# Kernel tuning notes

Hardware: AMD Instinct MI355X
Metric: run time of the kernel (lower is better)

Reference implementation:

```python
import jax, jax.numpy as jnp
import numpy as np

D, M, R, N = 64, 256, 3, 1024
L_MID = 2  # number of middle phi layers (L=4 total)


def sp10(x):
    # torch.nn.Softplus(beta=10)
    return jax.nn.softplus(10.0 * x) / 10.0


def setup_inputs() -> dict:
    key = jax.random.key(0)
    ks = jax.random.split(key, 16)
    w_scale = 1.0 / np.sqrt(R)
    a_ht_scale = 0.1 / np.sqrt(M)
    inp = {
        "X": jax.random.uniform(ks[0], (N, D), dtype=jnp.float32),
        "w_first": 1.0 * jax.random.normal(ks[1], (D, M, 1, R), dtype=jnp.float32),
        "w_mid": w_scale * jax.random.normal(ks[2], (L_MID, D, M, R, R), dtype=jnp.float32),
        "w_last": w_scale * jax.random.normal(ks[3], (D, M, R, 1), dtype=jnp.float32),
        "b_first": 0.1 * jax.random.normal(ks[4], (D, M, R), dtype=jnp.float32),
        "b_mid": 0.1 * jax.random.normal(ks[5], (L_MID, D, M, R), dtype=jnp.float32),
        "b_last": 0.1 * jax.random.normal(ks[6], (D, M, 1), dtype=jnp.float32),
        "a_first": jax.random.normal(ks[7], (D, M, R), dtype=jnp.float32),
        "a_mid": jax.random.normal(ks[8], (L_MID, D, M, R), dtype=jnp.float32),
    }
    # HT mixing matrices: init m*eye(m) per group (as in source) + small noise
    dims = [32, 16, 8, 4, 2]
    for i, g in enumerate(dims):
        eye = M * jnp.eye(M, dtype=jnp.float32)
        inp[f"aHT{i}"] = jnp.tile(eye[None], (g, 1, 1)) + 0.01 * jax.random.normal(ks[9 + i], (g, M, M), dtype=jnp.float32)
    inp["aHT5"] = a_ht_scale * jax.random.normal(ks[15], (1, M, 1), dtype=jnp.float32)
    return inp


def _layer(phis, phidots, w, b, a):
    # one hidden layer of the per-(d,m) rank-r MLP chain
    W = sp10(w)                                            # (d,m,k,l) >= 0
    z = jnp.einsum('ndmk,dmkl->ndml', phis, W) + b         # affine
    tz = jnp.tanh(z)
    ta = jnp.tanh(a)
    phidots = jnp.einsum('ndmk,dmkl->ndml', phidots, W) * (1.0 + ta * (1.0 - tz * tz))
    phis = z + tz * ta
    return phis, phidots


def _forward(X, w_first, w_mid, w_last, b_first, b_mid, b_last, a_first, a_mid,
             aHT0, aHT1, aHT2, aHT3, aHT4, aHT5):
    n = X.shape[0]
    phis = jnp.broadcast_to(X[:, :, None, None], (n, D, M, 1))  # expand_X
    phidots = jnp.ones_like(phis)
    phis, phidots = _layer(phis, phidots, w_first, b_first, a_first)
    for i in range(w_mid.shape[0]):
        phis, phidots = _layer(phis, phidots, w_mid[i], b_mid[i], a_mid[i])
    Wl = sp10(w_last)
    z = jnp.einsum('ndmk,dmkl->ndml', phis, Wl) + b_last   # (n,d,m,1)
    s = jax.nn.sigmoid(z)
    phidots = (jnp.einsum('ndmk,dmkl->ndml', phidots, Wl) * (s * (1.0 - s)))[..., 0]  # (n,d,m)
    # HT contraction: default couplings = consecutive pairs, d=64 -> 6 levels
    T = phidots
    for a in (aHT0, aHT1, aHT2, aHT3, aHT4, aHT5):
        nn_, dim, m_ = T.shape
        T = T.reshape(nn_, dim // 2, 2, m_).prod(axis=2)   # product over each pair
        A = sp10(a)
        A = A / A.sum(axis=1, keepdims=True)               # column-normalized nonneg mix
        T = jnp.einsum('ngm,gmk->ngk', T, A)
    return T[:, 0, 0]                                      # likelihood, shape (n,)


def reference(X, w_first, w_mid, w_last, b_first, b_mid, b_last, a_first, a_mid,
              aHT0, aHT1, aHT2, aHT3, aHT4, aHT5):
    return _forward(X, w_first, w_mid, w_last, b_first, b_mid, b_last,
                    a_first, a_mid, aHT0, aHT1, aHT2, aHT3, aHT4, aHT5)
```

## Files before the change

### kernel.cpp

```cpp
#include <hip/hip_runtime.h>
#include <cstdint>
#include <cstddef>

#define D_DIM 64
#define M_DIM 256
#define N_PTS 1024

typedef __attribute__((ext_vector_type(4))) float f32x4;
typedef __attribute__((ext_vector_type(2))) float f32x2;
typedef __attribute__((ext_vector_type(8))) short s16x8;

static __device__ __forceinline__ f32x2 pkfma(f32x2 a, f32x2 b, f32x2 c) {
#if __has_builtin(__builtin_elementwise_fma)
    return __builtin_elementwise_fma(a, b, c);
#else
    f32x2 r; r.x = fmaf(a.x, b.x, c.x); r.y = fmaf(a.y, b.y, c.y); return r;
#endif
}
static __device__ __forceinline__ f32x2 sp2(float s) {
    f32x2 r; r.x = s; r.y = s; return r;
}

static __device__ __forceinline__ float sp10f(float x) {
    float t = 10.f * x;
    return 0.1f * (fmaxf(t, 0.f) + log1pf(__expf(-fabsf(t))));
}

static __device__ __forceinline__ f32x2 ftanh2(f32x2 x) {
    f32x2 xs = x * sp2(2.88539008177793f);
    f32x2 e;
    e.x = __builtin_amdgcn_exp2f(xs.x);
    e.y = __builtin_amdgcn_exp2f(xs.y);
    f32x2 ep = e + sp2(1.f);
    f32x2 r;
    r.x = __builtin_amdgcn_rcpf(ep.x);
    r.y = __builtin_amdgcn_rcpf(ep.y);
    return pkfma(sp2(-2.f), r, sp2(1.f));
}

static __device__ __forceinline__ unsigned short f2bf(float x) {
    unsigned u = __float_as_uint(x);
    u = u + 0x7FFFu + ((u >> 16) & 1u);
    return (unsigned short)(u >> 16);
}
static __device__ __forceinline__ float bf2f(unsigned short h) {
    return __uint_as_float(((unsigned)h) << 16);
}

static __device__ __forceinline__ void split1(float x, unsigned& uh, unsigned& ul) {
    unsigned u = __float_as_uint(x);
    uh = u + 0x7FFFu + ((u >> 16) & 1u);
    ul = __float_as_uint(x - __uint_as_float(uh & 0xFFFF0000u));
}

static __device__ __forceinline__ const float* map_g(int g, const float* a0, const float* a1,
                                                     const float* a2, const float* a3,
                                                     const float* a4, int& lg) {
    if (g < 32) { lg = g;      return a0; }
    if (g < 48) { lg = g - 32; return a1; }
    if (g < 56) { lg = g - 48; return a2; }
    if (g < 60) { lg = g - 56; return a3; }
    lg = g - 60; return a4;
}

__global__ __launch_bounds__(256) void k_prep3(
    const float* __restrict__ X, const float* __restrict__ wf,
    const float* __restrict__ wm, const float* __restrict__ wl,
    const float* __restrict__ b1, const float* __restrict__ bm,
    const float* __restrict__ bl, const float* __restrict__ af,
    const float* __restrict__ am,
    const float* __restrict__ a0, const float* __restrict__ a1,
    const float* __restrict__ a2, const float* __restrict__ a3,
    const float* __restrict__ a4,
    float* __restrict__ Wpack, float* __restrict__ Xt,
    unsigned short* __restrict__ Anth, unsigned short* __restrict__ Antl) {
    __shared__ float tile[64][65];
    const int t = threadIdx.x;
    const int b = blockIdx.x;
    if (b < 16) {
        const int n0 = b * 64;
#pragma unroll
        for (int i = 0; i < 4; i++) {
            const int f   = i * 256 + t;
            const int row = f >> 4;
            const int c4  = f & 15;
            float4 v = *(const float4*)(X + (size_t)(n0 + row) * 64 + c4 * 4);
            tile[row][c4 * 4 + 0] = v.x;
            tile[row][c4 * 4 + 1] = v.y;
            tile[row][c4 * 4 + 2] = v.z;
            tile[row][c4 * 4 + 3] = v.w;
        }
        __syncthreads();
#pragma unroll
        for (int i = 0; i < 4; i++) {
            const int f    = i * 256 + t;
            const int drow = f >> 4;
            const int c4   = f & 15;
            float4 v;
            v.x = tile[c4 * 4 + 0][drow];
            v.y = tile[c4 * 4 + 1][drow];
            v.z = tile[c4 * 4 + 2][drow];
            v.w = tile[c4 * 4 + 3][drow];
            *(float4*)(Xt + (size_t)drow * 1024 + n0 + c4 * 4) = v;
        }
        return;
    }
    if (b < 80) {
        const int id = (b - 16) * 256 + t;
        float r[48];
#pragma unroll
        for (int q = 0; q < 48; q++) r[q] = 0.f;
#pragma unroll
        for (int q = 0; q < 3; q++) {
            r[0 + q] = sp10f(wf[id * 3 + q]);
            r[3 + q] = b1[id * 3 + q];
            r[6 + q] = tanhf(af[id * 3 + q]);
            r[39 + q] = sp10f(wl[id * 3 + q]);
        }
#pragma unroll
        for (int l = 0; l < 2; l++) {
            const size_t b9 = ((size_t)l * 16384 + id) * 9;
            const size_t b3 = ((size_t)l * 16384 + id) * 3;
#pragma unroll
            for (int q = 0; q < 9; q++) r[9 + l * 15 + q] = sp10f(wm[b9 + q]);
#pragma unroll
            for (int q = 0; q < 3; q++) {
                r[18 + l * 15 + q] = bm[b3 + q];
                r[21 + l * 15 + q] = tanhf(am[b3 + q]);
            }
        }
        r[42] = bl[id];
        float4* o = (float4*)(Wpack + (size_t)id * 48);
#pragma unroll
        for (int q = 0; q < 12; q++) o[q] = ((float4*)r)[q];
        return;
    }
    const int idx = b - 80;
    const int g   = idx >> 4;
    const int rr  = idx & 15;
    const int m0  = (rr & 3) * 64;
    const int k0  = (rr >> 2) * 64;
    int lg;
    const float* A  = map_g(g, a0, a1, a2, a3, a4, lg);
    const float* Ag = A + (size_t)lg * 65536;

#pragma unroll
    for (int i = 0; i < 4; i++) {
        const int f   = i * 256 + t;
        const int row = f >> 4;
        const int c4  = f & 15;
        float4 v = *(const float4*)(Ag + (size_t)(m0 + row) * 256 + k0 + c4 * 4);
        tile[row][c4 * 4 + 0] = v.x;
        tile[row][c4 * 4 + 1] = v.y;
        tile[row][c4 * 4 + 2] = v.z;
        tile[row][c4 * 4 + 3] = v.w;
    }
    __syncthreads();

#pragma unroll
    for (int i = 0; i < 4; i++) {
        const int f    = i * 256 + t;
        const int krow = f >> 4;
        const int c4   = f & 15;
        float v0 = sp10f(tile[c4 * 4 + 0][krow]);
        float v1 = sp10f(tile[c4 * 4 + 1][krow]);
        float v2 = sp10f(tile[c4 * 4 + 2][krow]);
        float v3 = sp10f(tile[c4 * 4 + 3][krow]);
        unsigned short h0 = f2bf(v0), h1 = f2bf(v1), h2 = f2bf(v2), h3 = f2bf(v3);
        ushort4 hi, lo;
        hi.x = h0; hi.y = h1; hi.z = h2; hi.w = h3;
        lo.x = f2bf(v0 - bf2f(h0));
        lo.y = f2bf(v1 - bf2f(h1));
        lo.z = f2bf(v2 - bf2f(h2));
        lo.w = f2bf(v3 - bf2f(h3));
        const size_t dst = (size_t)g * 65536 + (size_t)(k0 + krow) * 256 + m0 + c4 * 4;
        *(ushort4*)(Anth + dst) = hi;
        *(ushort4*)(Antl + dst) = lo;
    }
}

__global__ void k_csum_t(const unsigned short* __restrict__ Anth,
                         const unsigned short* __restrict__ Antl,
                         float* __restrict__ csum) {
    const int g    = blockIdx.x;
    const int w    = threadIdx.x >> 6;
    const int lane = threadIdx.x & 63;
    const int k    = blockIdx.y * 4 + w;
    const size_t base = (size_t)g * 65536 + k * 256 + lane * 4;
    uint2 vh = *(const uint2*)(Anth + base);
    uint2 vl = *(const uint2*)(Antl + base);
    float s = 0.f;
    s += bf2f((unsigned short)(vh.x & 0xFFFFu)) + bf2f((unsigned short)(vh.x >> 16));
    s += bf2f((unsigned short)(vh.y & 0xFFFFu)) + bf2f((unsigned short)(vh.y >> 16));
    s += bf2f((unsigned short)(vl.x & 0xFFFFu)) + bf2f((unsigned short)(vl.x >> 16));
    s += bf2f((unsigned short)(vl.y & 0xFFFFu)) + bf2f((unsigned short)(vl.y >> 16));
    for (int off = 32; off > 0; off >>= 1) s += __shfl_down(s, off);
    if (lane == 0) csum[g * 256 + k] = s;
}

__global__ __launch_bounds__(512, 1) void k_phase1(
    const float* __restrict__ Xt, const float* __restrict__ Wpack,
    unsigned short* __restrict__ P0h, unsigned short* __restrict__ P0l) {
    __shared__ float sT[128][33];
    __shared__ float sXd[2][256];
    const int j  = blockIdx.x;
    const int mc = blockIdx.y;
    const int n0 = blockIdx.z * 256;
    const int t  = threadIdx.x;
    const int w    = __builtin_amdgcn_readfirstlane(t >> 6);
    const int lane = t & 63;

    sXd[t >> 8][t & 255] = Xt[(size_t)(2 * j + (t >> 8)) * 1024 + n0 + (t & 255)];
    __syncthreads();

    f32x2 x[2][2];
#pragma unroll
    for (int e = 0; e < 2; e++) {
        x[e][0].x = sXd[e][lane];       x[e][0].y = sXd[e][64 + lane];
        x[e][1].x = sXd[e][128 + lane]; x[e][1].y = sXd[e][192 + lane];
    }

    const f32x2 one2 = sp2(1.f);
    f32x2 pB[4];

#pragma unroll 1
    for (int i = 0; i < 4; i++) {
        const int mm = w * 4 + i;
        const int m  = mc * 32 + mm;
        const float* __restrict__ rp0 =
            Wpack + (size_t)(((2 * j) << 8) + m) * 48;
        const float* __restrict__ rp1 = rp0 + 256 * 48;

        float W1a[2][3], B1a[2][3], T1a[2][3], Wm[2][2][9], Bm[2][2][3],
              Tm[2][2][3], Wla[2][3], Bla[2];
#pragma unroll
        for (int e = 0; e < 2; e++) {
            const float* __restrict__ rp = e ? rp1 : rp0;
#pragma unroll
            for (int r = 0; r < 3; r++) {
                W1a[e][r] = rp[r];
                B1a[e][r] = rp[3 + r];
                T1a[e][r] = rp[6 + r];
                Bm[e][0][r] = rp[18 + r];
                Tm[e][0][r] = rp[21 + r];
                Bm[e][1][r] = rp[33 + r];
                Tm[e][1][r] = rp[36 + r];
                Wla[e][r] = rp[39 + r];
            }
#pragma unroll
            for (int q = 0; q < 9; q++) {
                Wm[e][0][q] = rp[9 + q];
                Wm[e][1][q] = rp[24 + q];
            }
            Bla[e] = rp[42];
        }

        f32x2 phi[2][2][3], pd[2][2][3];
#pragma unroll
        for (int r = 0; r < 3; r++)
#pragma unroll
            for (int e = 0; e < 2; e++)
#pragma unroll
                for (int h = 0; h < 2; h++) {
                    f32x2 z  = pkfma(x[e][h], sp2(W1a[e][r]), sp2(B1a[e][r]));
                    f32x2 tz = ftanh2(z);
                    f32x2 ta = sp2(T1a[e][r]);
                    pd[e][h][r]  = sp2(W1a[e][r]) * pkfma(ta, pkfma(-tz, tz, one2), one2);
                    phi[e][h][r] = pkfma(tz, ta, z);
                }
#pragma unroll
        for (int l = 0; l < 2; l++) {
            f32x2 nphi[2][2][3], npd[2][2][3];
#pragma unroll
            for (int q = 0; q < 3; q++)
#pragma unroll
                for (int e = 0; e < 2; e++)
#pragma unroll
                    for (int h = 0; h < 2; h++) {
                        f32x2 z  = sp2(Bm[e][l][q]);
                        f32x2 dp = sp2(0.f);
#pragma unroll
                        for (int r = 0; r < 3; r++) {
                            f32x2 wv = sp2(Wm[e][l][r * 3 + q]);
                            z  = pkfma(phi[e][h][r], wv, z);
                            dp = pkfma(pd[e][h][r],  wv, dp);
                        }
                        f32x2 tz = ftanh2(z);
                        f32x2 ta = sp2(Tm[e][l][q]);
                        nphi[e][h][q] = pkfma(tz, ta, z);
                        npd[e][h][q]  = dp * pkfma(ta, pkfma(-tz, tz, one2), one2);
                    }
#pragma unroll
            for (int q = 0; q < 3; q++)
#pragma unroll
                for (int e = 0; e < 2; e++)
#pragma unroll
                    for (int h = 0; h < 2; h++) {
                        phi[e][h][q] = nphi[e][h][q];
                        pd[e][h][q]  = npd[e][h][q];
                    }
        }
        f32x2 prod[2][2];
#pragma unroll
        for (int e = 0; e < 2; e++)
#pragma unroll
            for (int h = 0; h < 2; h++) {
                f32x2 z  = sp2(Bla[e]);
                f32x2 dp = sp2(0.f);
#pragma unroll
                for (int r = 0; r < 3; r++) {
                    f32x2 wv = sp2(Wla[e][r]);
                    z  = pkfma(phi[e][h][r], wv, z);
                    dp = pkfma(pd[e][h][r],  wv, dp);
                }
                f32x2 zs = z * sp2(-1.4426950408889634f);
                f32x2 s;
                s.x = __builtin_amdgcn_rcpf(1.f + __builtin_amdgcn_exp2f(zs.x));
                s.y = __builtin_amdgcn_rcpf(1.f + __builtin_amdgcn_exp2f(zs.y));
                prod[e][h] = dp * s * (one2 - s);
            }
        f32x2 pA = prod[0][0] * prod[1][0];
        pB[i]    = prod[0][1] * prod[1][1];
        sT[lane][mm]      = pA.x;
        sT[64 + lane][mm] = pA.y;
    }
    __syncthreads();

    const size_t base = ((size_t)j * N_PTS + n0) * M_DIM + mc * 32;
#pragma unroll
    for (int it = 0; it < 2; it++) {
        const int idx = it * 512 + t;
        const int row = idx >> 3;
        const int c4  = idx & 7;
        float4 v;
        v.x = sT[row][c4 * 4 + 0];
        v.y = sT[row][c4 * 4 + 1];
        v.z = sT[row][c4 * 4 + 2];
        v.w = sT[row][c4 * 4 + 3];
        unsigned uh0, ul0, uh1, ul1, uh2, ul2, uh3, ul3;
        split1(v.x, uh0, ul0);
        split1(v.y, uh1, ul1);
        split1(v.z, uh2, ul2);
        split1(v.w, uh3, ul3);
        uint2 hp, lp;
        hp.x = __builtin_amdgcn_perm(uh1, uh0, 0x07060302u);
        hp.y = __builtin_amdgcn_perm(uh3, uh2, 0x07060302u);
        lp.x = __builtin_amdgcn_perm(ul1, ul0, 0x07060302u);
        lp.y = __builtin_amdgcn_perm(ul3, ul2, 0x07060302u);
        *(uint2*)(P0h + base + (size_t)row * M_DIM + c4 * 4) = hp;
        *(uint2*)(P0l + base + (size_t)row * M_DIM + c4 * 4) = lp;
    }
    __syncthreads();

#pragma unroll
    for (int i = 0; i < 4; i++) {
        const int mm = w * 4 + i;
        sT[lane][mm]      = pB[i].x;
        sT[64 + lane][mm] = pB[i].y;
    }
    __syncthreads();
    const size_t base2 = base + (size_t)128 * M_DIM;
#pragma unroll
    for (int it = 0; it < 2; it++) {
        const int idx = it * 512 + t;
        const int row = idx >> 3;
        const int c4  = idx & 7;
        float4 v;
        v.x = sT[row][c4 * 4 + 0];
        v.y = sT[row][c4 * 4 + 1];
        v.z = sT[row][c4 * 4 + 2];
        v.w = sT[row][c4 * 4 + 3];
        unsigned uh0, ul0, uh1, ul1, uh2, ul2, uh3, ul3;
        split1(v.x, uh0, ul0);
        split1(v.y, uh1, ul1);
        split1(v.z, uh2, ul2);
        split1(v.w, uh3, ul3);
        uint2 hp, lp;
        hp.x = __builtin_amdgcn_perm(uh1, uh0, 0x07060302u);
        hp.y = __builtin_amdgcn_perm(uh3, uh2, 0x07060302u);
        lp.x = __builtin_amdgcn_perm(ul1, ul0, 0x07060302u);
        lp.y = __builtin_amdgcn_perm(ul3, ul2, 0x07060302u);
        *(uint2*)(P0h + base2 + (size_t)row * M_DIM + c4 * 4) = hp;
        *(uint2*)(P0l + base2 + (size_t)row * M_DIM + c4 * 4) = lp;
    }
}

#define LDST64 72

__global__ __launch_bounds__(256, 4) void k_g64ps(
    const unsigned short* __restrict__ Th, const unsigned short* __restrict__ Tl,
    const unsigned short* __restrict__ Bh, const unsigned short* __restrict__ Bl,
    const float* __restrict__ csum, float* __restrict__ Tout) {
    __shared__ unsigned short sAh[64 * LDST64];
    __shared__ unsigned short sAl[64 * LDST64];
    __shared__ unsigned short sBh[64 * LDST64];
    __shared__ unsigned short sBl[64 * LDST64];

    const int g  = blockIdx.z;
    const int n0 = blockIdx.x * 64;
    const int k0 = blockIdx.y * 64;
    const unsigned short* Thg = Th + (size_t)g * N_PTS * 256;
    const unsigned short* Tlg = Tl + (size_t)g * N_PTS * 256;
    const unsigned short* Bhg = Bh + (size_t)g * 65536;
    const unsigned short* Blg = Bl + (size_t)g * 65536;

    const int tid  = threadIdx.x;
    const int lane = tid & 63;
    const int w    = tid >> 6;
    const int wr   = w >> 1;
    const int wc   = w & 1;
    const int lr   = lane & 15;
    const int lk   = lane >> 4;

    f32x4 acc[2][2];
#pragma unroll
    for (int a = 0; a < 2; a++)
#pragma unroll
        for (int b = 0; b < 2; b++) acc[a][b] = (f32x4){0.f, 0.f, 0.f, 0.f};

    for (int kb = 0; kb < 256; kb += 64) {
#pragma unroll
        for (int i = 0; i < 2; i++) {
            const int idx = i * 256 + tid;
            const int row = idx >> 3;
            const int seg = idx & 7;
            const size_t srcA = (size_t)(n0 + row) * 256 + kb + seg * 8;
            const size_t srcB = (size_t)(k0 + row) * 256 + kb + seg * 8;
            *(uint4*)&sAh[row * LDST64 + seg * 8] = *(const uint4*)(Thg + srcA);
            *(uint4*)&sAl[row * LDST64 + seg * 8] = *(const uint4*)(Tlg + srcA);
            *(uint4*)&sBh[row * LDST64 + seg * 8] = *(const uint4*)(Bhg + srcB);
            *(uint4*)&sBl[row * LDST64 + seg * 8] = *(const uint4*)(Blg + srcB);
        }
        __syncthreads();

        s16x8 ah[2][2], al[2][2], bh[2][2], bl[2][2];
#pragma unroll
        for (int nt = 0; nt < 2; nt++)
#pragma unroll
            for (int ks = 0; ks < 2; ks++) {
                const int off = (wr * 32 + nt * 16 + lr) * LDST64 + ks * 32 + lk * 8;
                ah[nt][ks] = *(const s16x8*)&sAh[off];
                al[nt][ks] = *(const s16x8*)&sAl[off];
            }
#pragma unroll
        for (int kt = 0; kt < 2; kt++)
#pragma unroll
            for (int ks = 0; ks < 2; ks++) {
                const int off = (wc * 32 + kt * 16 + lr) * LDST64 + ks * 32 + lk * 8;
                bh[kt][ks] = *(const s16x8*)&sBh[off];
                bl[kt][ks] = *(const s16x8*)&sBl[off];
            }
#pragma unroll
        for (int ks = 0; ks < 2; ks++)
#pragma unroll
            for (int nt = 0; nt < 2; nt++)
#pragma unroll
                for (int kt = 0; kt < 2; kt++) {
                    acc[nt][kt] = __builtin_amdgcn_mfma_f32_16x16x32_bf16(ah[nt][ks], bh[kt][ks], acc[nt][kt], 0, 0, 0);
                    acc[nt][kt] = __builtin_amdgcn_mfma_f32_16x16x32_bf16(ah[nt][ks], bl[kt][ks], acc[nt][kt], 0, 0, 0);
                    acc[nt][kt] = __builtin_amdgcn_mfma_f32_16x16x32_bf16(al[nt][ks], bh[kt][ks], acc[nt][kt], 0, 0, 0);
                }
        __syncthreads();
    }

    float* Og = Tout + (size_t)g * N_PTS * 256;
#pragma unroll
    for (int kt = 0; kt < 2; kt++) {
        const int col = k0 + wc * 32 + kt * 16 + lr;
        const float inv = 1.0f / csum[g * 256 + col];
#pragma unroll
        for (int nt = 0; nt < 2; nt++) {
            const int rbase = n0 + wr * 32 + nt * 16 + lk * 4;
#pragma unroll
            for (int r = 0; r < 4; r++)
                Og[(size_t)(rbase + r) * 256 + col] = acc[nt][kt][r] * inv;
        }
    }
}

__global__ __launch_bounds__(256, 4) void k_gemm64(const float* __restrict__ Tin,
                                                   const unsigned short* __restrict__ Bh,
                                                   const unsigned short* __restrict__ Bl,
                                                   const float* __restrict__ csum,
                                                   float* __restrict__ Tout) {
    __shared__ unsigned short sAh[64 * LDST64];
    __shared__ unsigned short sAl[64 * LDST64];
    __shared__ unsigned short sBh[64 * LDST64];
    __shared__ unsigned short sBl[64 * LDST64];

    const int g  = blockIdx.z;
    const int n0 = blockIdx.x * 64;
    const int k0 = blockIdx.y * 64;
    const float* T0  = Tin + (size_t)(2 * g) * N_PTS * 256;
    const float* T1p = T0 + (size_t)N_PTS * 256;
    const unsigned short* Bhg = Bh + (size_t)g * 65536;
    const unsigned short* Blg = Bl + (size_t)g * 65536;

    const int tid  = threadIdx.x;
    const int lane = tid & 63;
    const int w    = tid >> 6;
    const int wr   = w >> 1;
    const int wc   = w & 1;
    const int lr   = lane & 15;
    const int lk   = lane >> 4;

    f32x4 acc[2][2];
#pragma unroll
    for (int a = 0; a < 2; a++)
#pragma unroll
        for (int b = 0; b < 2; b++) acc[a][b] = (f32x4){0.f, 0.f, 0.f, 0.f};

    for (int kb = 0; kb < 256; kb += 64) {
#pragma unroll
        for (int i = 0; i < 4; i++) {
            const int idx = i * 256 + tid;
            const int row = idx >> 4;
            const int c4  = idx & 15;
            float4 v = *(const float4*)(T0 + (size_t)(n0 + row) * 256 + kb + c4 * 4);
            float4 u = *(const float4*)(T1p + (size_t)(n0 + row) * 256 + kb + c4 * 4);
            v.x *= u.x; v.y *= u.y; v.z *= u.z; v.w *= u.w;
            unsigned uh0, ul0, uh1, ul1, uh2, ul2, uh3, ul3;
            split1(v.x, uh0, ul0);
            split1(v.y, uh1, ul1);
            split1(v.z, uh2, ul2);
            split1(v.w, uh3, ul3);
            uint2 hp, lp;
            hp.x = __builtin_amdgcn_perm(uh1, uh0, 0x07060302u);
            hp.y = __builtin_amdgcn_perm(uh3, uh2, 0x07060302u);
            lp.x = __builtin_amdgcn_perm(ul1, ul0, 0x07060302u);
            lp.y = __builtin_amdgcn_perm(ul3, ul2, 0x07060302u);
            *(uint2*)&sAh[row * LDST64 + c4 * 4] = hp;
            *(uint2*)&sAl[row * LDST64 + c4 * 4] = lp;
        }
#pragma unroll
        for (int i = 0; i < 2; i++) {
            const int idx = i * 256 + tid;
            const int row = idx >> 3;
            const int seg = idx & 7;
            const size_t src = (size_t)(k0 + row) * 256 + kb + seg * 8;
            *(uint4*)&sBh[row * LDST64 + seg * 8] = *(const uint4*)(Bhg + src);
            *(uint4*)&sBl[row * LDST64 + seg * 8] = *(const uint4*)(Blg + src);
        }
        __syncthreads();

        s16x8 ah[2][2], al[2][2], bh[2][2], bl[2][2];
#pragma unroll
        for (int nt = 0; nt < 2; nt++)
#pragma unroll
            for (int ks = 0; ks < 2; ks++) {
                const int off = (wr * 32 + nt * 16 + lr) * LDST64 + ks * 32 + lk * 8;
                ah[nt][ks] = *(const s16x8*)&sAh[off];
                al[nt][ks] = *(const s16x8*)&sAl[off];
            }
#pragma unroll
        for (int kt = 0; kt < 2; kt++)
#pragma unroll
            for (int ks = 0; ks < 2; ks++) {
                const int off = (wc * 32 + kt * 16 + lr) * LDST64 + ks * 32 + lk * 8;
                bh[kt][ks] = *(const s16x8*)&sBh[off];
                bl[kt][ks] = *(const s16x8*)&sBl[off];
            }
#pragma unroll
        for (int ks = 0; ks < 2; ks++)
#pragma unroll
            for (int nt = 0; nt < 2; nt++)
#pragma unroll
                for (int kt = 0; kt < 2; kt++) {
                    acc[nt][kt] = __builtin_amdgcn_mfma_f32_16x16x32_bf16(ah[nt][ks], bh[kt][ks], acc[nt][kt], 0, 0, 0);
                    acc[nt][kt] = __builtin_amdgcn_mfma_f32_16x16x32_bf16(ah[nt][ks], bl[kt][ks], acc[nt][kt], 0, 0, 0);
                    acc[nt][kt] = __builtin_amdgcn_mfma_f32_16x16x32_bf16(al[nt][ks], bh[kt][ks], acc[nt][kt], 0, 0, 0);
                }
        __syncthreads();
    }

    float* Og = Tout + (size_t)g * N_PTS * 256;
#pragma unroll
    for (int kt = 0; kt < 2; kt++) {
        const int col = k0 + wc * 32 + kt * 16 + lr;
        const float inv = 1.0f / csum[g * 256 + col];
#pragma unroll
        for (int nt = 0; nt < 2; nt++) {
            const int rbase = n0 + wr * 32 + nt * 16 + lk * 4;
#pragma unroll
            for (int r = 0; r < 4; r++)
                Og[(size_t)(rbase + r) * 256 + col] = acc[nt][kt][r] * inv;
        }
    }
}

__global__ void k_l5(const float* __restrict__ Tin, const float* __restrict__ a5,
                     float* __restrict__ out) {
    const int n = blockIdx.x;
    const int m = threadIdx.x;
    __shared__ float sv[256], sw[256];
    float w = sp10f(a5[m]);
    float v = Tin[(size_t)n * 256 + m] * Tin[(size_t)(N_PTS + n) * 256 + m] * w;
    sv[m] = v;
    sw[m] = w;
    __syncthreads();
    for (int s = 128; s > 0; s >>= 1) {
        if (m < s) { sv[m] += sv[m + s]; sw[m] += sw[m + s]; }
        __syncthreads();
    }
    if (m == 0) out[n] = sv[0] / sw[0];
}

extern "C" void kernel_launch(void* const* d_in, const int* in_sizes, int n_in,
                              void* d_out, int out_size, void* d_ws, size_t ws_size,
                              hipStream_t stream) {
    const float* X  = (const float*)d_in[0];
    const float* wf = (const float*)d_in[1];
    const float* wm = (const float*)d_in[2];
    const float* wl = (const float*)d_in[3];
    const float* b1 = (const float*)d_in[4];
    const float* bm = (const float*)d_in[5];
    const float* bl = (const float*)d_in[6];
    const float* af = (const float*)d_in[7];
    const float* am = (const float*)d_in[8];
    const float* a0 = (const float*)d_in[9];
    const float* a1 = (const float*)d_in[10];
    const float* a2 = (const float*)d_in[11];
    const float* a3 = (const float*)d_in[12];
    const float* a4 = (const float*)d_in[13];
    const float* a5 = (const float*)d_in[14];
    float* out = (float*)d_out;

    float* ws    = (float*)d_ws;
    float* Wpack = ws;
    float* Xt    = Wpack + 786432;
    float* csum  = Xt + 65536;
    unsigned short* Anth = (unsigned short*)(csum + 15872);
    unsigned short* Antl = Anth + (size_t)62 * 65536;
    float* B0    = (float*)(Antl + (size_t)62 * 65536);
    float* B1    = B0 + (size_t)32 * N_PTS * M_DIM;
    unsigned short* P0h = (unsigned short*)B1;
    unsigned short* P0l = P0h + (size_t)32 * N_PTS * M_DIM;

    k_prep3<<<1072, 256, 0, stream>>>(X, wf, wm, wl, b1, bm, bl, af, am,
                                      a0, a1, a2, a3, a4, Wpack, Xt, Anth, Antl);
    k_csum_t<<<dim3(62, 64), 256, 0, stream>>>(Anth, Antl, csum);
    k_phase1<<<dim3(32, 8, 4), 512, 0, stream>>>(Xt, Wpack, P0h, P0l);

    k_g64ps<<<dim3(16, 4, 32), 256, 0, stream>>>(P0h, P0l, Anth, Antl, csum, B0);
    k_gemm64<<<dim3(16, 4, 16), 256, 0, stream>>>(B0, Anth + (size_t)32 * 65536,
                                                  Antl + (size_t)32 * 65536, csum + 32 * 256, B1);
    k_gemm64<<<dim3(16, 4, 8), 256, 0, stream>>>(B1, Anth + (size_t)48 * 65536,
                                                 Antl + (size_t)48 * 65536, csum + 48 * 256, B0);
    k_gemm64<<<dim3(16, 4, 4), 256, 0, stream>>>(B0, Anth + (size_t)56 * 65536,
                                                 Antl + (size_t)56 * 65536, csum + 56 * 256, B1);
    k_gemm64<<<dim3(16, 4, 2), 256, 0, stream>>>(B1, Anth + (size_t)60 * 65536,
                                                 Antl + (size_t)60 * 65536, csum + 60 * 256, B0);
    k_l5<<<N_PTS, 256, 0, stream>>>(B0, a5, out);
}
```

Measured before the change: 146.6 us.

## Split pair-product into separate kernel and load MFMA operands directly from global

Each HT level's fused product, bf16 split and GEMM kernel is replaced by a standalone elementwise pair/split kernel followed by a shared-memory-free GEMM. The GEMM reads MFMA fragments straight from global memory and drops both barriers. This removes LDS staging, sync overhead and the redundant per-tile recomputation of the product and split. In exchange it adds four extra kernel launches and an extra global round-trip of the split operands, and direct global fragment loads may be less coalesced.

After: 233.6 us. 1.59x slower.

```diff
diff --git a/kernel.cpp b/kernel.cpp
--- a/kernel.cpp
+++ b/kernel.cpp
@@ -385,24 +385,45 @@
     }
 }
 
-#define LDST64 72
-
-__global__ __launch_bounds__(256, 4) void k_g64ps(
+__global__ __launch_bounds__(256) void k_pair(const float* __restrict__ G,
+                                              unsigned short* __restrict__ Qh,
+                                              unsigned short* __restrict__ Ql) {
+    const int i = blockIdx.x * 256 + threadIdx.x;
+#pragma unroll
+    for (int s = 0; s < 2; s++) {
+        const int idx = i * 2 + s;
+        const int q = idx >> 16;
+        const int r = idx & 65535;
+        const float4 a = *(const float4*)(G + ((size_t)(2 * q) << 18) + r * 4);
+        const float4 b = *(const float4*)(G + ((size_t)(2 * q + 1) << 18) + r * 4);
+        float4 v;
+        v.x = a.x * b.x; v.y = a.y * b.y; v.z = a.z * b.z; v.w = a.w * b.w;
+        unsigned uh0, ul0, uh1, ul1, uh2, ul2, uh3, ul3;
+        split1(v.x, uh0, ul0);
+        split1(v.y, uh1, ul1);
+        split1(v.z, uh2, ul2);
+        split1(v.w, uh3, ul3);
+        uint2 hp, lp;
+        hp.x = __builtin_amdgcn_perm(uh1, uh0, 0x07060302u);
+        hp.y = __builtin_amdgcn_perm(uh3, uh2, 0x07060302u);
+        lp.x = __builtin_amdgcn_perm(ul1, ul0, 0x07060302u);
+        lp.y = __builtin_amdgcn_perm(ul3, ul2, 0x07060302u);
+        *(uint2*)(Qh + ((size_t)q << 18) + r * 4) = hp;
+        *(uint2*)(Ql + ((size_t)q << 18) + r * 4) = lp;
+    }
+}
+
+__global__ __launch_bounds__(256) void k_gdir(
     const unsigned short* __restrict__ Th, const unsigned short* __restrict__ Tl,
     const unsigned short* __restrict__ Bh, const unsigned short* __restrict__ Bl,
     const float* __restrict__ csum, float* __restrict__ Tout) {
-    __shared__ unsigned short sAh[64 * LDST64];
-    __shared__ unsigned short sAl[64 * LDST64];
-    __shared__ unsigned short sBh[64 * LDST64];
-    __shared__ unsigned short sBl[64 * LDST64];
-
     const int g  = blockIdx.z;
     const int n0 = blockIdx.x * 64;
     const int k0 = blockIdx.y * 64;
-    const unsigned short* Thg = Th + (size_t)g * N_PTS * 256;
-    const unsigned short* Tlg = Tl + (size_t)g * N_PTS * 256;
-    const unsigned short* Bhg = Bh + (size_t)g * 65536;
-    const unsigned short* Blg = Bl + (size_t)g * 65536;
+    const unsigned short* Thg = Th + ((size_t)g << 18);
+    const unsigned short* Tlg = Tl + ((size_t)g << 18);
+    const unsigned short* Bhg = Bh + ((size_t)g << 16);
+    const unsigned short* Blg = Bl + ((size_t)g << 16);
 
     const int tid  = threadIdx.x;
     const int lane = tid & 63;
@@ -412,168 +433,41 @@
     const int lr   = lane & 15;
     const int lk   = lane >> 4;
 
+    const int rowA = n0 + wr * 32 + lr;
+    const int rowB = k0 + wc * 32 + lr;
+
     f32x4 acc[2][2];
 #pragma unroll
     for (int a = 0; a < 2; a++)
 #pragma unroll
         for (int b = 0; b < 2; b++) acc[a][b] = (f32x4){0.f, 0.f, 0.f, 0.f};
 
-    for (int kb = 0; kb < 256; kb += 64) {
-#pragma unroll
-        for (int i = 0; i < 2; i++) {
-            const int idx = i * 256 + tid;
-            const int row = idx >> 3;
-            const int seg = idx & 7;
-            const size_t srcA = (size_t)(n0 + row) * 256 + kb + seg * 8;
-            const size_t srcB = (size_t)(k0 + row) * 256 + kb + seg * 8;
-            *(uint4*)&sAh[row * LDST64 + seg * 8] = *(const uint4*)(Thg + srcA);
-            *(uint4*)&sAl[row * LDST64 + seg * 8] = *(const uint4*)(Tlg + srcA);
-            *(uint4*)&sBh[row * LDST64 + seg * 8] = *(const uint4*)(Bhg + srcB);
-            *(uint4*)&sBl[row * LDST64 + seg * 8] = *(const uint4*)(Blg + srcB);
-        }
-        __syncthreads();
-
-        s16x8 ah[2][2], al[2][2], bh[2][2], bl[2][2];
+#pragma unroll
+    for (int kb = 0; kb < 256; kb += 32) {
+        s16x8 ah[2], al[2], bh[2], bl[2];
+#pragma unroll
+        for (int nt = 0; nt < 2; nt++) {
+            const size_t addr = (size_t)(rowA + nt * 16) * 256 + kb + lk * 8;
+            ah[nt] = *(const s16x8*)(Thg + addr);
+            al[nt] = *(const s16x8*)(Tlg + addr);
+        }
+#pragma unroll
+        for (int kt = 0; kt < 2; kt++) {
+            const size_t addr = (size_t)(rowB + kt * 16) * 256 + kb + lk * 8;
+            bh[kt] = *(const s16x8*)(Bhg + addr);
+            bl[kt] = *(const s16x8*)(Blg + addr);
+        }
 #pragma unroll
         for (int nt = 0; nt < 2; nt++)
 #pragma unroll
-            for (int ks = 0; ks < 2; ks++) {
-                const int off = (wr * 32 + nt * 16 + lr) * LDST64 + ks * 32 + lk * 8;
-                ah[nt][ks] = *(const s16x8*)&sAh[off];
-                al[nt][ks] = *(const s16x8*)&sAl[off];
+            for (int kt = 0; kt < 2; kt++) {
+                acc[nt][kt] = __builtin_amdgcn_mfma_f32_16x16x32_bf16(ah[nt], bh[kt], acc[nt][kt], 0, 0, 0);
+                acc[nt][kt] = __builtin_amdgcn_mfma_f32_16x16x32_bf16(ah[nt], bl[kt], acc[nt][kt], 0, 0, 0);
+                acc[nt][kt] = __builtin_amdgcn_mfma_f32_16x16x32_bf16(al[nt], bh[kt], acc[nt][kt], 0, 0, 0);
             }
-#pragma unroll
-        for (int kt = 0; kt < 2; kt++)
-#pragma unroll
-            for (int ks = 0; ks < 2; ks++) {
-                const int off = (wc * 32 + kt * 16 + lr) * LDST64 + ks * 32 + lk * 8;
-                bh[kt][ks] = *(const s16x8*)&sBh[off];
-                bl[kt][ks] = *(const s16x8*)&sBl[off];
-            }
-#pragma unroll
-        for (int ks = 0; ks < 2; ks++)
-#pragma unroll
-            for (int nt = 0; nt < 2; nt++)
-#pragma unroll
-                for (int kt = 0; kt < 2; kt++) {
-                    acc[nt][kt] = __builtin_amdgcn_mfma_f32_16x16x32_bf16(ah[nt][ks], bh[kt][ks], acc[nt][kt], 0, 0, 0);
-                    acc[nt][kt] = __builtin_amdgcn_mfma_f32_16x16x32_bf16(ah[nt][ks], bl[kt][ks], acc[nt][kt], 0, 0, 0);
-                    acc[nt][kt] = __builtin_amdgcn_mfma_f32_16x16x32_bf16(al[nt][ks], bh[kt][ks], acc[nt][kt], 0, 0, 0);
-                }
-        __syncthreads();
-    }
-
-    float* Og = Tout + (size_t)g * N_PTS * 256;
-#pragma unroll
-    for (int kt = 0; kt < 2; kt++) {
-        const int col = k0 + wc * 32 + kt * 16 + lr;
-        const float inv = 1.0f / csum[g * 256 + col];
-#pragma unroll
-        for (int nt = 0; nt < 2; nt++) {
-            const int rbase = n0 + wr * 32 + nt * 16 + lk * 4;
-#pragma unroll
-            for (int r = 0; r < 4; r++)
-                Og[(size_t)(rbase + r) * 256 + col] = acc[nt][kt][r] * inv;
-        }
-    }
-}
-
-__global__ __launch_bounds__(256, 4) void k_gemm64(const float* __restrict__ Tin,
-                                                   const unsigned short* __restrict__ Bh,
-                                                   const unsigned short* __restrict__ Bl,
-                                                   const float* __restrict__ csum,
-                                                   float* __restrict__ Tout) {
-    __shared__ unsigned short sAh[64 * LDST64];
-    __shared__ unsigned short sAl[64 * LDST64];
-    __shared__ unsigned short sBh[64 * LDST64];
-    __shared__ unsigned short sBl[64 * LDST64];
-
-    const int g  = blockIdx.z;
-    const int n0 = blockIdx.x * 64;
-    const int k0 = blockIdx.y * 64;
-    const float* T0  = Tin + (size_t)(2 * g) * N_PTS * 256;
-    const float* T1p = T0 + (size_t)N_PTS * 256;
-    const unsigned short* Bhg = Bh + (size_t)g * 65536;
-    const unsigned short* Blg = Bl + (size_t)g * 65536;
-
-    const int tid  = threadIdx.x;
-    const int lane = tid & 63;
-    const int w    = tid >> 6;
-    const int wr   = w >> 1;
-    const int wc   = w & 1;
-    const int lr   = lane & 15;
-    const int lk   = lane >> 4;
-
-    f32x4 acc[2][2];
-#pragma unroll
-    for (int a = 0; a < 2; a++)
-#pragma unroll
-        for (int b = 0; b < 2; b++) acc[a][b] = (f32x4){0.f, 0.f, 0.f, 0.f};
-
-    for (int kb = 0; kb < 256; kb += 64) {
-#pragma unroll
-        for (int i = 0; i < 4; i++) {
-            const int idx = i * 256 + tid;
-            const int row = idx >> 4;
-            const int c4  = idx & 15;
-            float4 v = *(const float4*)(T0 + (size_t)(n0 + row) * 256 + kb + c4 * 4);
-            float4 u = *(const float4*)(T1p + (size_t)(n0 + row) * 256 + kb + c4 * 4);
-            v.x *= u.x; v.y *= u.y; v.z *= u.z; v.w *= u.w;
-            unsigned uh0, ul0, uh1, ul1, uh2, ul2, uh3, ul3;
-            split1(v.x, uh0, ul0);
-            split1(v.y, uh1, ul1);
-            split1(v.z, uh2, ul2);
-            split1(v.w, uh3, ul3);
-            uint2 hp, lp;
-            hp.x = __builtin_amdgcn_perm(uh1, uh0, 0x07060302u);
-            hp.y = __builtin_amdgcn_perm(uh3, uh2, 0x07060302u);
-            lp.x = __builtin_amdgcn_perm(ul1, ul0, 0x07060302u);
-            lp.y = __builtin_amdgcn_perm(ul3, ul2, 0x07060302u);
-            *(uint2*)&sAh[row * LDST64 + c4 * 4] = hp;
-            *(uint2*)&sAl[row * LDST64 + c4 * 4] = lp;
-        }
-#pragma unroll
-        for (int i = 0; i < 2; i++) {
-            const int idx = i * 256 + tid;
-            const int row = idx >> 3;
-            const int seg = idx & 7;
-            const size_t src = (size_t)(k0 + row) * 256 + kb + seg * 8;
-            *(uint4*)&sBh[row * LDST64 + seg * 8] = *(const uint4*)(Bhg + src);
-            *(uint4*)&sBl[row * LDST64 + seg * 8] = *(const uint4*)(Blg + src);
-        }
-        __syncthreads();
-
-        s16x8 ah[2][2], al[2][2], bh[2][2], bl[2][2];
-#pragma unroll
-        for (int nt = 0; nt < 2; nt++)
-#pragma unroll
-            for (int ks = 0; ks < 2; ks++) {
-                const int off = (wr * 32 + nt * 16 + lr) * LDST64 + ks * 32 + lk * 8;
-                ah[nt][ks] = *(const s16x8*)&sAh[off];
-                al[nt][ks] = *(const s16x8*)&sAl[off];
-            }
-#pragma unroll
-        for (int kt = 0; kt < 2; kt++)
-#pragma unroll
-            for (int ks = 0; ks < 2; ks++) {
-                const int off = (wc * 32 + kt * 16 + lr) * LDST64 + ks * 32 + lk * 8;
-                bh[kt][ks] = *(const s16x8*)&sBh[off];
-                bl[kt][ks] = *(const s16x8*)&sBl[off];
-            }
-#pragma unroll
-        for (int ks = 0; ks < 2; ks++)
-#pragma unroll
-            for (int nt = 0; nt < 2; nt++)
-#pragma unroll
-                for (int kt = 0; kt < 2; kt++) {
-                    acc[nt][kt] = __builtin_amdgcn_mfma_f32_16x16x32_bf16(ah[nt][ks], bh[kt][ks], acc[nt][kt], 0, 0, 0);
-                    acc[nt][kt] = __builtin_amdgcn_mfma_f32_16x16x32_bf16(ah[nt][ks], bl[kt][ks], acc[nt][kt], 0, 0, 0);
-                    acc[nt][kt] = __builtin_amdgcn_mfma_f32_16x16x32_bf16(al[nt][ks], bh[kt][ks], acc[nt][kt], 0, 0, 0);
-                }
-        __syncthreads();
-    }
-
-    float* Og = Tout + (size_t)g * N_PTS * 256;
+    }
+
+    float* Og = Tout + ((size_t)g << 18);
 #pragma unroll
     for (int kt = 0; kt < 2; kt++) {
         const int col = k0 + wc * 32 + kt * 16 + lr;
@@ -631,24 +525,33 @@
     float* csum  = Xt + 65536;
     unsigned short* Anth = (unsigned short*)(csum + 15872);
     unsigned short* Antl = Anth + (size_t)62 * 65536;
-    float* B0    = (float*)(Antl + (size_t)62 * 65536);
-    float* B1    = B0 + (size_t)32 * N_PTS * M_DIM;
-    unsigned short* P0h = (unsigned short*)B1;
-    unsigned short* P0l = P0h + (size_t)32 * N_PTS * M_DIM;
+    unsigned short* P0h  = Antl + (size_t)62 * 65536;
+    unsigned short* P0l  = P0h + (size_t)32 * 262144;
+    float* Gbuf  = (float*)(P0l + (size_t)32 * 262144);
+    unsigned short* Qh   = (unsigned short*)(Gbuf + (size_t)32 * 262144);
+    unsigned short* Ql   = Qh + (size_t)16 * 262144;
 
     k_prep3<<<1072, 256, 0, stream>>>(X, wf, wm, wl, b1, bm, bl, af, am,
                                       a0, a1, a2, a3, a4, Wpack, Xt, Anth, Antl);
     k_csum_t<<<dim3(62, 64), 256, 0, stream>>>(Anth, Antl, csum);
     k_phase1<<<dim3(32, 8, 4), 512, 0, stream>>>(Xt, Wpack, P0h, P0l);
 
-    k_g64ps<<<dim3(16, 4, 32), 256, 0, stream>>>(P0h, P0l, Anth, Antl, csum, B0);
-    k_gemm64<<<dim3(16, 4, 16), 256, 0, stream>>>(B0, Anth + (size_t)32 * 65536,
-                                                  Antl + (size_t)32 * 65536, csum + 32 * 256, B1);
-    k_gemm64<<<dim3(16, 4, 8), 256, 0, stream>>>(B1, Anth + (size_t)48 * 65536,
-                                                 Antl + (size_t)48 * 65536, csum + 48 * 256, B0);
-    k_gemm64<<<dim3(16, 4, 4), 256, 0, stream>>>(B0, Anth + (size_t)56 * 65536,
-                                                 Antl + (size_t)56 * 65536, csum + 56 * 256, B1);
-    k_gemm64<<<dim3(16, 4, 2), 256, 0, stream>>>(B1, Anth + (size_t)60 * 65536,
-                                                 Antl + (size_t)60 * 65536, csum + 60 * 256, B0);
-    k_l5<<<N_PTS, 256, 0, stream>>>(B0, a5, out);
-}
+    k_gdir<<<dim3(16, 4, 32), 256, 0, stream>>>(P0h, P0l, Anth, Antl, csum, Gbuf);
+    k_pair<<<2048, 256, 0, stream>>>(Gbuf, Qh, Ql);
+    k_gdir<<<dim3(16, 4, 16), 256, 0, stream>>>(Qh, Ql, Anth + (size_t)32 * 65536,
+                                                Antl + (size_t)32 * 65536,
+                                                csum + 32 * 256, Gbuf);
+    k_pair<<<1024, 256, 0, stream>>>(Gbuf, Qh, Ql);
+    k_gdir<<<dim3(16, 4, 8), 256, 0, stream>>>(Qh, Ql, Anth + (size_t)48 * 65536,
+                                               Antl + (size_t)48 * 65536,
+                                               csum + 48 * 256, Gbuf);
+    k_pair<<<512, 256, 0, stream>>>(Gbuf, Qh, Ql);
+    k_gdir<<<dim3(16, 4, 4), 256, 0, stream>>>(Qh, Ql, Anth + (size_t)56 * 65536,
+                                               Antl + (size_t)56 * 65536,
+                                               csum + 56 * 256, Gbuf);
+    k_pair<<<256, 256, 0, stream>>>(Gbuf, Qh, Ql);
+    k_gdir<<<dim3(16, 4, 2), 256, 0, stream>>>(Qh, Ql, Anth + (size_t)60 * 65536,
+                                               Antl + (size_t)60 * 65536,
+                                               csum + 60 * 256, Gbuf);
+    k_l5<<<N_PTS, 256, 0, stream>>>(Gbuf, a5, out);
+}
```
